# Performance work log

Measured on AMD Instinct MI355X. Metric: run time of the kernel, lower is better.

The kernel has to match this reference:

```python
import jax, jax.numpy as jnp
import numpy as np

EMBED = 1024
HEADS = 16
HEAD_DIM = EMBED // HEADS
EPS = 1e-5  # torch LayerNorm default


def setup_inputs() -> dict:
    key = jax.random.key(0)
    ks = jax.random.split(key, 11)
    s = 1.0 / np.sqrt(EMBED)
    def lin(kw, kb):
        W = jax.random.uniform(kw, (EMBED, EMBED), jnp.float32, -s, s)
        b = jax.random.uniform(kb, (EMBED,), jnp.float32, -s, s)
        return W, b
    Wq, bq = lin(ks[0], ks[1])
    Wk, bk = lin(ks[2], ks[3])
    Wv, bv = lin(ks[4], ks[5])
    Wo, bo = lin(ks[6], ks[7])
    x = jax.random.normal(ks[8], (2, 2048, EMBED), jnp.float32)
    gamma = jnp.ones((EMBED,), jnp.float32)
    beta = jnp.zeros((EMBED,), jnp.float32)
    return {"x": x, "Wq": Wq, "bq": bq, "Wk": Wk, "bk": bk,
            "Wv": Wv, "bv": bv, "Wo": Wo, "bo": bo,
            "gamma": gamma, "beta": beta}


def _attn(x, Wq, bq, Wk, bk, Wv, bv, Wo, bo, gamma, beta):
    N, S, _ = x.shape
    # torch Linear: y = x @ W.T + b
    q = (x @ Wq.T + bq).reshape(N, S, HEADS, HEAD_DIM).transpose(0, 2, 1, 3)
    k = (x @ Wk.T + bk).reshape(N, S, HEADS, HEAD_DIM).transpose(0, 2, 1, 3)
    v = (x @ Wv.T + bv).reshape(N, S, HEADS, HEAD_DIM).transpose(0, 2, 1, 3)
    energy = jnp.einsum("bhqd,bhkd->bhqk", q, k) / np.sqrt(HEAD_DIM)
    causal = jnp.tril(jnp.ones((S, S), bool))  # [S,S]
    energy = jnp.where(causal[None, None], energy, -jnp.inf)
    attn = jax.nn.softmax(energy, axis=-1)
    out = jnp.einsum("bhqk,bhkd->bhqd", attn, v)
    out = out.transpose(0, 2, 1, 3).reshape(N, S, EMBED)
    out = out @ Wo.T + bo
    # residual + LayerNorm
    h = out + x
    mu = jnp.mean(h, axis=-1, keepdims=True)
    var = jnp.var(h, axis=-1, keepdims=True)
    return (h - mu) * jax.lax.rsqrt(var + EPS) * gamma + beta


def reference(x, Wq, bq, Wk, bk, Wv, bv, Wo, bo, gamma, beta):
    return _attn(x, Wq, bq, Wk, bk, Wv, bv, Wo, bo, gamma, beta)
```

## Files before the change

### kernel.cpp

```cpp
#include <hip/hip_runtime.h>

typedef __attribute__((ext_vector_type(8))) short short8;
typedef __attribute__((ext_vector_type(4))) float f32x4;
typedef __attribute__((ext_vector_type(4))) short short4v;

template<bool B> struct BoolC { static constexpr bool value = B; };

__device__ __forceinline__ short f2bs(float f) {
    union { float f; unsigned u; } c; c.f = f;
    unsigned r = 0x7FFFu + ((c.u >> 16) & 1u);
    return (short)((c.u + r) >> 16);
}

__device__ __forceinline__ unsigned fbits(float f) {
    union { float f; unsigned u; } c; c.f = f; return c.u;
}

__device__ __forceinline__ void gld_lds16(const void* g, void* l) {
    __builtin_amdgcn_global_load_lds(
        (const __attribute__((address_space(1))) unsigned int*)g,
        (__attribute__((address_space(3))) unsigned int*)l, 16, 0, 0);
}

__device__ __forceinline__ f32x4 mfma16(short8 a, short8 b, f32x4 c) {
    return __builtin_amdgcn_mfma_f32_16x16x32_bf16(a, b, c, 0, 0, 0);
}

__global__ __launch_bounds__(256) void cvtall_kernel(
    const float* __restrict__ x,
    const float* __restrict__ Wq, const float* __restrict__ Wk,
    const float* __restrict__ Wv, const float* __restrict__ Wo,
    short* __restrict__ xb, short* __restrict__ wqkv, short* __restrict__ wob)
{
    int i = blockIdx.x * 256 + threadIdx.x;
    const float* src; short* dst; int off;
    if (i < 1048576) { src = x; dst = xb; off = i; }
    else {
        int j = i - 1048576, which = j >> 18;
        off = j & 262143;
        src = which == 0 ? Wq : (which == 1 ? Wk : (which == 2 ? Wv : Wo));
        dst = which == 3 ? wob : (wqkv + (size_t)which * 1048576);
    }
    float4 v = ((const float4*)src)[off];
    short4v o;
    o.x = f2bs(v.x); o.y = f2bs(v.y); o.z = f2bs(v.z); o.w = f2bs(v.w);
    ((short4v*)dst)[off] = o;
}

#define BN 128
#define BK 32

template<int MODE, int BMt>
__global__ __launch_bounds__(256) void gemm_bt(
    const short* __restrict__ A, const short* __restrict__ B,
    int M, int N, int K,
    const float* __restrict__ b0, const float* __restrict__ b1, const float* __restrict__ b2,
    short* __restrict__ oq, short* __restrict__ ok_, short* __restrict__ ov,
    const float* __restrict__ bo, const float* __restrict__ xres,
    float* __restrict__ outf)
{
    constexpr int IM = BMt / 32;
    __shared__ __align__(16) short As[2][BMt * BK];
    __shared__ __align__(16) short Bs[2][BN * BK];
    const int tid = threadIdx.x;
    const int wave = tid >> 6, lane = tid & 63;
    const int lhi = lane >> 4, llo = lane & 15;
    const int row0 = blockIdx.x * BMt, col0 = blockIdx.y * BN;
    const int wr = (wave >> 1) * (BMt / 2), wc = (wave & 1) * 64;

    f32x4 acc[IM][4] = {};

    const short* gA0 = A + (size_t)(row0 + (tid >> 2)) * K + (tid & 3) * 8;
    const short* gA1 = A + (size_t)(row0 + 64 + (tid >> 2)) * K + (tid & 3) * 8;
    const short* gB0 = B + (size_t)(col0 + (tid >> 2)) * K + (tid & 3) * 8;
    const short* gB1 = B + (size_t)(col0 + 64 + (tid >> 2)) * K + (tid & 3) * 8;

    auto stage = [&](int kk, int bf) {
        gld_lds16(gA0 + kk, &As[bf][wave * 512]);
        if constexpr (BMt == 128) gld_lds16(gA1 + kk, &As[bf][2048 + wave * 512]);
        gld_lds16(gB0 + kk, &Bs[bf][wave * 512]);
        gld_lds16(gB1 + kk, &Bs[bf][2048 + wave * 512]);
    };

    const int NT = K / BK;
    stage(0, 0);
    __syncthreads();

    int bf = 0;
    for (int kt = 0; kt < NT; ++kt) {
        if (kt + 1 < NT) stage((kt + 1) * BK, bf ^ 1);
        short8 af[IM], bfr[4];
        #pragma unroll
        for (int i = 0; i < IM; ++i)
            af[i] = *(const short8*)&As[bf][(wr + i * 16 + llo) * BK + lhi * 8];
        #pragma unroll
        for (int j = 0; j < 4; ++j)
            bfr[j] = *(const short8*)&Bs[bf][(wc + j * 16 + llo) * BK + lhi * 8];
        #pragma unroll
        for (int i = 0; i < IM; ++i)
            #pragma unroll
            for (int j = 0; j < 4; ++j)
                acc[i][j] = mfma16(af[i], bfr[j], acc[i][j]);
        if (kt + 1 < NT) __syncthreads();
        bf ^= 1;
    }

    if constexpr (MODE == 0) {
        const int which = (int)blockIdx.y >> 3;
        if (which < 2) {
            const float* bia = which == 0 ? b0 : b1;
            short* dst = which == 0 ? oq : ok_;
            #pragma unroll
            for (int i = 0; i < IM; ++i)
                #pragma unroll
                for (int j = 0; j < 4; ++j)
                    #pragma unroll
                    for (int r = 0; r < 4; ++r) {
                        int m = row0 + wr + i * 16 + lhi * 4 + r;
                        int nn = (col0 & 1023) + wc + j * 16 + llo;
                        float v = acc[i][j][r] + bia[nn];
                        int h = nn >> 6, d = nn & 63;
                        int bb = m >> 11, s = m & 2047;
                        dst[((size_t)((bb * 16 + h) * 2048 + s)) * 64 + d] = f2bs(v);
                    }
        } else {
            __shared__ __align__(16) short Ts[4 * 64 * 26];
            short* T = Ts + wave * (64 * 26);
            const int nn0 = (col0 - 2048) + wc;
            const int h = nn0 >> 6;
            const int bb = row0 >> 11;
            const int s0 = (row0 & 2047) + wr;
            short* vdst = ov + ((size_t)(bb * 16 + h) * 64) * 2048;
            #pragma unroll
            for (int i = 0; i < IM; ++i) {
                #pragma unroll
                for (int j = 0; j < 4; ++j) {
                    const float bias = b2[nn0 + j * 16 + llo];
                    unsigned u01 = __builtin_amdgcn_perm(fbits(acc[i][j][1] + bias),
                                                         fbits(acc[i][j][0] + bias), 0x07060302u);
                    unsigned u23 = __builtin_amdgcn_perm(fbits(acc[i][j][3] + bias),
                                                         fbits(acc[i][j][2] + bias), 0x07060302u);
                    unsigned* Tw = (unsigned*)&T[(j * 16 + llo) * 26];
                    Tw[lhi * 2]     = u01;
                    Tw[lhi * 2 + 1] = u23;
                }
                short8 a0 = *(const short8*)&T[lane * 26];
                short8 a1 = *(const short8*)&T[lane * 26 + 8];
                *(short8*)&vdst[(size_t)lane * 2048 + s0 + i * 16]     = a0;
                *(short8*)&vdst[(size_t)lane * 2048 + s0 + i * 16 + 8] = a1;
            }
        }
    } else {
        #pragma unroll
        for (int i = 0; i < IM; ++i)
            #pragma unroll
            for (int j = 0; j < 4; ++j)
                #pragma unroll
                for (int r = 0; r < 4; ++r) {
                    int m = row0 + wr + i * 16 + lhi * 4 + r;
                    int n = col0 + wc + j * 16 + llo;
                    size_t idx = (size_t)m * N + n;
                    outf[idx] = acc[i][j][r] + bo[n] + xres[idx];
                }
    }
}

#define SCL 0.18033688011f

__global__ __launch_bounds__(256) void attn_kernel(
    const short* __restrict__ Q, const short* __restrict__ K,
    const short* __restrict__ Vt, short* __restrict__ O)
{
    const int id = blockIdx.x;
    const int u = id >> 3;
    const int bh = (id & 7) * 4 + (u & 3);
    const int s4 = u >> 2;
    const int p = (s4 < 8) ? (2 * s4) : (31 - 2 * s4);
    const int q0L = p * 64, q0H = (31 - p) * 64;
    const int ntH = 32 - p;

    const short* Qb = Q  + (size_t)bh * 2048 * 64;
    const short* Kb = K  + (size_t)bh * 2048 * 64;
    const short* Vb = Vt + (size_t)bh * 64 * 2048;

    __shared__ __align__(16) short Ks[2][64 * 64];
    __shared__ __align__(16) short Vs[2][64 * 64];
    __shared__ __align__(16) short Ps[4][2][16 * 68];

    const int tid = threadIdx.x, wave = tid >> 6, lane = tid & 63;
    const int lhi = lane >> 4, llo = lane & 15;
    const int qwL = q0L + wave * 16, qwH = q0H + wave * 16;
    const int qgL = qwL + llo, qgH = qwH + llo;

    auto scale8 = [](short8 a) {
        short8 r;
        #pragma unroll
        for (int i = 0; i < 8; ++i) {
            union { unsigned u; float f; } c; c.u = ((unsigned)(unsigned short)a[i]) << 16;
            r[i] = f2bs(c.f * SCL);
        }
        return r;
    };
    const short8 qfL0 = scale8(*(const short8*)&Qb[(size_t)(qwL + llo) * 64 + lhi * 8]);
    const short8 qfL1 = scale8(*(const short8*)&Qb[(size_t)(qwL + llo) * 64 + 32 + lhi * 8]);
    const short8 qfH0 = scale8(*(const short8*)&Qb[(size_t)(qwH + llo) * 64 + lhi * 8]);
    const short8 qfH1 = scale8(*(const short8*)&Qb[(size_t)(qwH + llo) * 64 + 32 + lhi * 8]);

    const int tr = tid >> 3, tc = tid & 7, sc = tc ^ (tr & 7);
    const short* kS0 = Kb + (size_t)tr * 64 + sc * 8;
    const short* kS1 = Kb + (size_t)(32 + tr) * 64 + sc * 8;
    const short* vS0 = Vb + (size_t)tr * 2048 + sc * 8;
    const short* vS1 = Vb + (size_t)(32 + tr) * 2048 + sc * 8;
    const int dOff = wave * 512;

    f32x4 oL[4] = {}, oH[4] = {};
    float lL = 0.f, lH = 0.f;

    unsigned* PwH = (unsigned*)Ps[wave][0] + llo * 34;
    unsigned* PwL = (unsigned*)Ps[wave][1] + llo * 34;

    gld_lds16(kS0, Ks[0] + dOff);
    gld_lds16(kS1, Ks[0] + 2048 + dOff);
    gld_lds16(vS0, Vs[0] + dOff);
    gld_lds16(vS1, Vs[0] + 2048 + dOff);
    __syncthreads();

    const int swq = (llo & 7) << 3;

    auto smx = [&](f32x4 (&st)[4], float& lrow, unsigned* Pw, int qg, int kk0, bool diag) {
        if (diag) {
            #pragma unroll
            for (int t = 0; t < 4; ++t)
                #pragma unroll
                for (int j = 0; j < 4; ++j)
                    if (kk0 + t * 16 + lhi * 4 + j > qg) st[t][j] = -1e30f;
        }
        float rs0 = 0.f, rs1 = 0.f;
        #pragma unroll
        for (int t = 0; t < 4; ++t) {
            st[t][0] = exp2f(st[t][0]);
            st[t][1] = exp2f(st[t][1]);
            st[t][2] = exp2f(st[t][2]);
            st[t][3] = exp2f(st[t][3]);
            rs0 += st[t][0] + st[t][2];
            rs1 += st[t][1] + st[t][3];
        }
        lrow += rs0 + rs1;
        #pragma unroll
        for (int t = 0; t < 4; ++t) {
            Pw[t * 8 + lhi * 2]     = __builtin_amdgcn_perm(fbits(st[t][1]), fbits(st[t][0]), 0x07060302u);
            Pw[t * 8 + lhi * 2 + 1] = __builtin_amdgcn_perm(fbits(st[t][3]), fbits(st[t][2]), 0x07060302u);
        }
    };

    int cur = 0;
    auto tile = [&](int kt, auto dualc) {
        constexpr bool DUAL = decltype(dualc)::value;
        const int kk0 = kt * 64;
        if (kt + 1 < ntH) {
            const int nk = kk0 + 64;
            gld_lds16(kS0 + (size_t)nk * 64, Ks[cur ^ 1] + dOff);
            gld_lds16(kS1 + (size_t)nk * 64, Ks[cur ^ 1] + 2048 + dOff);
            gld_lds16(vS0 + nk, Vs[cur ^ 1] + dOff);
            gld_lds16(vS1 + nk, Vs[cur ^ 1] + 2048 + dOff);
        }

        f32x4 stH[4], stL[4];
        __builtin_amdgcn_s_setprio(1);
        #pragma unroll
        for (int t = 0; t < 4; ++t) {
            const int row = t * 16 + llo;
            short8 kf0 = *(const short8*)&Ks[cur][row * 64 + ((lhi * 8) ^ swq)];
            short8 kf1 = *(const short8*)&Ks[cur][row * 64 + ((lhi * 8 + 32) ^ swq)];
            f32x4 a = {};
            a = mfma16(kf0, qfH0, a);
            stH[t] = mfma16(kf1, qfH1, a);
            if (DUAL) {
                f32x4 b = {};
                b = mfma16(kf0, qfL0, b);
                stL[t] = mfma16(kf1, qfL1, b);
            }
        }
        __builtin_amdgcn_s_setprio(0);

        smx(stH, lH, PwH, qgH, kk0, kt == ntH - 1);
        if (DUAL) smx(stL, lL, PwL, qgL, kk0, kt == p);

        const short8 pH0 = *(const short8*)&Ps[wave][0][llo * 68 + lhi * 8];
        const short8 pH1 = *(const short8*)&Ps[wave][0][llo * 68 + 32 + lhi * 8];
        short8 pL0, pL1;
        if (DUAL) {
            pL0 = *(const short8*)&Ps[wave][1][llo * 68 + lhi * 8];
            pL1 = *(const short8*)&Ps[wave][1][llo * 68 + 32 + lhi * 8];
        }
        __builtin_amdgcn_s_setprio(1);
        #pragma unroll
        for (int dt = 0; dt < 4; ++dt) {
            const int row = dt * 16 + llo;
            short8 vf0 = *(const short8*)&Vs[cur][row * 64 + ((lhi * 8) ^ swq)];
            short8 vf1 = *(const short8*)&Vs[cur][row * 64 + ((lhi * 8 + 32) ^ swq)];
            oH[dt] = mfma16(pH0, vf0, oH[dt]);
            oH[dt] = mfma16(pH1, vf1, oH[dt]);
            if (DUAL) {
                oL[dt] = mfma16(pL0, vf0, oL[dt]);
                oL[dt] = mfma16(pL1, vf1, oL[dt]);
            }
        }
        __builtin_amdgcn_s_setprio(0);

        if (kt + 1 < ntH) __syncthreads();
        cur ^= 1;
    };

    for (int kt = 0; kt <= p; ++kt)      tile(kt, BoolC<true>{});
    for (int kt = p + 1; kt < ntH; ++kt) tile(kt, BoolC<false>{});

    lH += __shfl_xor(lH, 16); lH += __shfl_xor(lH, 32);
    lL += __shfl_xor(lL, 16); lL += __shfl_xor(lL, 32);
    const int b = bh >> 4, h = bh & 15;
    const float invH = 1.f / lH, invL = 1.f / lL;
    #pragma unroll
    for (int j = 0; j < 4; ++j) {
        const float ivH = __shfl(invH, lhi * 4 + j);
        const float ivL = __shfl(invL, lhi * 4 + j);
        const size_t rowH = (size_t)(b * 2048 + qwH + lhi * 4 + j);
        const size_t rowL = (size_t)(b * 2048 + qwL + lhi * 4 + j);
        #pragma unroll
        for (int dt = 0; dt < 4; ++dt) {
            int d = dt * 16 + llo;
            O[rowH * 1024 + h * 64 + d] = f2bs(oH[dt][j] * ivH);
            O[rowL * 1024 + h * 64 + d] = f2bs(oL[dt][j] * ivL);
        }
    }
}

__global__ __launch_bounds__(256) void ln_kernel(float* __restrict__ out,
        const float* __restrict__ gamma, const float* __restrict__ beta)
{
    const int row = blockIdx.x;
    float* p = out + (size_t)row * 1024;
    const int tid = threadIdx.x;
    float4 v = ((const float4*)p)[tid];
    float s = v.x + v.y + v.z + v.w;
    float ss = v.x * v.x + v.y * v.y + v.z * v.z + v.w * v.w;
    #pragma unroll
    for (int d = 1; d < 64; d <<= 1) {
        s  += __shfl_xor(s, d);
        ss += __shfl_xor(ss, d);
    }
    __shared__ float red[8];
    const int wave = tid >> 6, lane = tid & 63;
    if (lane == 0) { red[wave] = s; red[4 + wave] = ss; }
    __syncthreads();
    s  = red[0] + red[1] + red[2] + red[3];
    ss = red[4] + red[5] + red[6] + red[7];
    const float mu = s * (1.0f / 1024.0f);
    const float var = ss * (1.0f / 1024.0f) - mu * mu;
    const float rstd = rsqrtf(var + 1e-5f);
    float4 g = ((const float4*)gamma)[tid];
    float4 b = ((const float4*)beta)[tid];
    v.x = (v.x - mu) * rstd * g.x + b.x;
    v.y = (v.y - mu) * rstd * g.y + b.y;
    v.z = (v.z - mu) * rstd * g.z + b.z;
    v.w = (v.w - mu) * rstd * g.w + b.w;
    ((float4*)p)[tid] = v;
}

extern "C" void kernel_launch(void* const* d_in, const int* in_sizes, int n_in,
                              void* d_out, int out_size, void* d_ws, size_t ws_size,
                              hipStream_t stream)
{
    const float* x  = (const float*)d_in[0];
    const float* Wq = (const float*)d_in[1];
    const float* bq = (const float*)d_in[2];
    const float* Wk = (const float*)d_in[3];
    const float* bk = (const float*)d_in[4];
    const float* Wv = (const float*)d_in[5];
    const float* bv = (const float*)d_in[6];
    const float* Wo = (const float*)d_in[7];
    const float* bo = (const float*)d_in[8];
    const float* gamma = (const float*)d_in[9];
    const float* beta  = (const float*)d_in[10];
    float* out = (float*)d_out;

    char* ws = (char*)d_ws;
    short* xb   = (short*)(ws);
    short* wqkv = (short*)(ws + (8ull  << 20));
    short* wob  = (short*)(ws + (14ull << 20));
    short* qb   = (short*)(ws + (16ull << 20));
    short* kb   = (short*)(ws + (24ull << 20));
    short* vtb  = (short*)(ws + (32ull << 20));
    short* ab   = xb;

    cvtall_kernel<<<8192, 256, 0, stream>>>(x, Wq, Wk, Wv, Wo, xb, wqkv, wob);

    gemm_bt<0, 128><<<dim3(32, 24), 256, 0, stream>>>(xb, wqkv, 4096, 3072, 1024,
        bq, bk, bv, qb, kb, vtb, nullptr, nullptr, nullptr);

    attn_kernel<<<512, 256, 0, stream>>>(qb, kb, vtb, ab);

    gemm_bt<1, 64><<<dim3(64, 8), 256, 0, stream>>>(ab, wob, 4096, 1024, 1024,
        nullptr, nullptr, nullptr, nullptr, nullptr, nullptr, bo, x, out);

    ln_kernel<<<4096, 256, 0, stream>>>(out, gamma, beta);
}
```

Measured before the change: 133.8 us.

## Triple-buffer GEMM LDS staging with vmcnt waits and a single barrier

Replaces the double-buffered A/B shared tiles in the bf16 GEMM with a three-slot ring buffer that prefetches two K-tiles ahead. Each iteration waits on outstanding global-to-LDS loads with explicit s_waitcnt vmcnt counts plus one s_barrier, instead of a full __syncthreads after every step. The V-transpose scratch is aliased onto the same shared buffer behind an added barrier, which keeps shared-memory use down. This aims to hide more global load latency, but it depends on the hand-picked vmcnt values matching the number of loads per stage.

```diff
diff --git a/kernel.cpp b/kernel.cpp
--- a/kernel.cpp
+++ b/kernel.cpp
@@ -24,6 +24,12 @@
 
 __device__ __forceinline__ f32x4 mfma16(short8 a, short8 b, f32x4 c) {
     return __builtin_amdgcn_mfma_f32_16x16x32_bf16(a, b, c, 0, 0, 0);
+}
+
+template<int N> __device__ __forceinline__ void vmwait() {
+    if constexpr (N == 0)      asm volatile("s_waitcnt vmcnt(0)" ::: "memory");
+    else if constexpr (N == 3) asm volatile("s_waitcnt vmcnt(3)" ::: "memory");
+    else if constexpr (N == 4) asm volatile("s_waitcnt vmcnt(4)" ::: "memory");
 }
 
 __global__ __launch_bounds__(256) void cvtall_kernel(
@@ -60,8 +66,9 @@
     float* __restrict__ outf)
 {
     constexpr int IM = BMt / 32;
-    __shared__ __align__(16) short As[2][BMt * BK];
-    __shared__ __align__(16) short Bs[2][BN * BK];
+    constexpr int BUFSZ = (BMt + BN) * BK;
+    constexpr int LPS = (BMt == 128) ? 4 : 3;
+    __shared__ __align__(16) short SM[3 * BUFSZ];
     const int tid = threadIdx.x;
     const int wave = tid >> 6, lane = tid & 63;
     const int lhi = lane >> 4, llo = lane & 15;
@@ -76,33 +83,40 @@
     const short* gB1 = B + (size_t)(col0 + 64 + (tid >> 2)) * K + (tid & 3) * 8;
 
     auto stage = [&](int kk, int bf) {
-        gld_lds16(gA0 + kk, &As[bf][wave * 512]);
-        if constexpr (BMt == 128) gld_lds16(gA1 + kk, &As[bf][2048 + wave * 512]);
-        gld_lds16(gB0 + kk, &Bs[bf][wave * 512]);
-        gld_lds16(gB1 + kk, &Bs[bf][2048 + wave * 512]);
+        short* As = SM + bf * BUFSZ;
+        short* Bs = As + BMt * BK;
+        gld_lds16(gA0 + kk, &As[wave * 512]);
+        if constexpr (BMt == 128) gld_lds16(gA1 + kk, &As[2048 + wave * 512]);
+        gld_lds16(gB0 + kk, &Bs[wave * 512]);
+        gld_lds16(gB1 + kk, &Bs[2048 + wave * 512]);
     };
 
     const int NT = K / BK;
     stage(0, 0);
-    __syncthreads();
-
-    int bf = 0;
+    stage(BK, 1);
+
     for (int kt = 0; kt < NT; ++kt) {
-        if (kt + 1 < NT) stage((kt + 1) * BK, bf ^ 1);
+        if (kt < NT - 1) vmwait<LPS>(); else vmwait<0>();
+        __builtin_amdgcn_s_barrier();
+        __builtin_amdgcn_sched_barrier(0);
+        if (kt + 2 < NT) {
+            int b2i = kt + 2; b2i -= (b2i >= 3) ? 3 : 0; b2i -= (b2i >= 3) ? 3 : 0;
+            stage((kt + 2) * BK, (kt + 2) % 3);
+        }
+        const short* As = SM + (kt % 3) * BUFSZ;
+        const short* Bs = As + BMt * BK;
         short8 af[IM], bfr[4];
         #pragma unroll
         for (int i = 0; i < IM; ++i)
-            af[i] = *(const short8*)&As[bf][(wr + i * 16 + llo) * BK + lhi * 8];
+            af[i] = *(const short8*)&As[(wr + i * 16 + llo) * BK + lhi * 8];
         #pragma unroll
         for (int j = 0; j < 4; ++j)
-            bfr[j] = *(const short8*)&Bs[bf][(wc + j * 16 + llo) * BK + lhi * 8];
+            bfr[j] = *(const short8*)&Bs[(wc + j * 16 + llo) * BK + lhi * 8];
         #pragma unroll
         for (int i = 0; i < IM; ++i)
             #pragma unroll
             for (int j = 0; j < 4; ++j)
                 acc[i][j] = mfma16(af[i], bfr[j], acc[i][j]);
-        if (kt + 1 < NT) __syncthreads();
-        bf ^= 1;
     }
 
     if constexpr (MODE == 0) {
@@ -124,8 +138,8 @@
                         dst[((size_t)((bb * 16 + h) * 2048 + s)) * 64 + d] = f2bs(v);
                     }
         } else {
-            __shared__ __align__(16) short Ts[4 * 64 * 26];
-            short* T = Ts + wave * (64 * 26);
+            __syncthreads();
+            short* T = SM + wave * (64 * 26);
             const int nn0 = (col0 - 2048) + wc;
             const int h = nn0 >> 6;
             const int bb = row0 >> 11;
```

Result: faster. 117.5 us (-12.2%).
